# Kernel tuning notes

Hardware: AMD Instinct MI355X
Metric: run time of the kernel (lower is better)

## Reference

```python
import jax, jax.numpy as jnp
import numpy as np

SEQ = 4096
HIDDEN = 4096
HEAD_DIM = 1024
NUM_HEAD = HIDDEN // HEAD_DIM  # 4


def setup_inputs() -> dict:
    key = jax.random.key(0)
    ks = jax.random.split(key, 7)
    scale = 1.0 / np.sqrt(HIDDEN)  # torch Linear default-ish init scale
    h = jax.random.normal(ks[0], (SEQ, HIDDEN), dtype=jnp.float32)
    Wq = jax.random.normal(ks[1], (NUM_HEAD, HIDDEN, HEAD_DIM), dtype=jnp.float32) * scale
    bq = jax.random.normal(ks[2], (NUM_HEAD, HEAD_DIM), dtype=jnp.float32) * scale
    Wk = jax.random.normal(ks[3], (NUM_HEAD, HIDDEN, HEAD_DIM), dtype=jnp.float32) * scale
    bk = jax.random.normal(ks[4], (NUM_HEAD, HEAD_DIM), dtype=jnp.float32) * scale
    Wv = jax.random.normal(ks[5], (NUM_HEAD, HIDDEN, HEAD_DIM), dtype=jnp.float32) * scale
    bv = jax.random.normal(ks[6], (NUM_HEAD, HEAD_DIM), dtype=jnp.float32) * scale
    return {"h": h, "Wq": Wq, "bq": bq, "Wk": Wk, "bk": bk, "Wv": Wv, "bv": bv}


def reference(h, Wq, bq, Wk, bk, Wv, bv):
    # Batched per-head projections: q/k/v [H, S, E]
    q = jnp.einsum('sd,hde->hse', h, Wq) + bq[:, None, :]
    k = jnp.einsum('sd,hde->hse', h, Wk) + bk[:, None, :]
    v = jnp.einsum('sd,hde->hse', h, Wv) + bv[:, None, :]
    # Full (non-causal) attention scores [H, S, S], scaled by sqrt(head_dim)
    s = jnp.einsum('hse,hte->hst', q, k) / jnp.sqrt(jnp.asarray(HEAD_DIM, h.dtype))
    p = jax.nn.softmax(s, axis=-1)
    out = jnp.einsum('hst,hte->hse', p, v)  # [H, S, E]
    # Concatenate heads along feature dim -> [S, H*E]
    return jnp.transpose(out, (1, 0, 2)).reshape(h.shape[0], -1)
```

## Files before the change

kernel.cpp:

```cpp
#include <hip/hip_runtime.h>

#define SEQ   4096
#define HID   4096
#define EDIM  1024
#define NHEAD 4

typedef __attribute__((ext_vector_type(8))) short short8;
typedef __attribute__((ext_vector_type(4))) float f32x4;

typedef const __attribute__((address_space(1))) void* gas_ptr;
typedef __attribute__((address_space(3))) void* las_ptr;
#define GLD16(g, l) __builtin_amdgcn_global_load_lds((gas_ptr)(g), (las_ptr)(l), 16, 0, 0)

#define BARRIER() __builtin_amdgcn_s_barrier()
#define SCHED0()  __builtin_amdgcn_sched_barrier(0)

__device__ __forceinline__ unsigned short f2bf(float f) {
  union { float f; unsigned u; } v; v.f = f;
  unsigned r = v.u + 0x7fffu + ((v.u >> 16) & 1u);
  return (unsigned short)(r >> 16);
}
__device__ __forceinline__ float bf2f(unsigned short u) {
  union { unsigned u; float f; } v; v.u = ((unsigned)u) << 16;
  return v.f;
}

__global__ __launch_bounds__(256) void hconv_kernel(const float* __restrict__ in,
                                                    unsigned short* __restrict__ out) {
  size_t i = ((size_t)blockIdx.x * 256 + threadIdx.x) * 8;
  const float4 a = *(const float4*)(in + i);
  const float4 b = *(const float4*)(in + i + 4);
  short8 o;
  o[0] = (short)f2bf(a.x); o[1] = (short)f2bf(a.y);
  o[2] = (short)f2bf(a.z); o[3] = (short)f2bf(a.w);
  o[4] = (short)f2bf(b.x); o[5] = (short)f2bf(b.y);
  o[6] = (short)f2bf(b.z); o[7] = (short)f2bf(b.w);
  *(short8*)(out + i) = o;
}

__global__ __launch_bounds__(256) void wconv_kernel(const float* __restrict__ Wq,
                                                    const float* __restrict__ Wk,
                                                    const float* __restrict__ Wv,
                                                    unsigned short* __restrict__ wt) {
  const int mh = blockIdx.y;
  const int mat = mh >> 2, head = mh & 3;
  const float* W = (mat == 0 ? Wq : (mat == 1 ? Wk : Wv)) + (size_t)head * HID * EDIM;
  unsigned short* out = wt + (size_t)mh * EDIM * HID;
  const int tile = blockIdx.x;
  const int td = tile >> 4;
  const int te = tile & 15;
  __shared__ float lds[64][65];
  const int tid = threadIdx.x;
  const int r = tid >> 4, c4 = (tid & 15) * 4;
#pragma unroll
  for (int it = 0; it < 4; ++it) {
    int dr = r + 16 * it;
    const float4 v = *(const float4*)&W[(size_t)(td * 64 + dr) * EDIM + te * 64 + c4];
    lds[dr][c4 + 0] = v.x; lds[dr][c4 + 1] = v.y;
    lds[dr][c4 + 2] = v.z; lds[dr][c4 + 3] = v.w;
  }
  __syncthreads();
#pragma unroll
  for (int it = 0; it < 4; ++it) {
    int er = r + 16 * it;
    ushort4 o;
    o.x = f2bf(lds[c4 + 0][er]); o.y = f2bf(lds[c4 + 1][er]);
    o.z = f2bf(lds[c4 + 2][er]); o.w = f2bf(lds[c4 + 3][er]);
    *(ushort4*)&out[(size_t)(te * 64 + er) * HID + td * 64 + c4] = o;
  }
}

template <int MODE>
__global__ __launch_bounds__(512, 2) void gemm256_kernel(
    const unsigned short* __restrict__ Aall, const unsigned short* __restrict__ Ball,
    long long aBatch, long long bBatch, int K,
    const float* __restrict__ biasAll, long long biasBatch,
    void* __restrict__ outAll, long long outBatch, int ldOut, float scale,
    int gx, int gxy) {
  extern __shared__ char smem[];

  const int nwg = (int)gridDim.x;
  const int lin = (int)blockIdx.x;
  int wg = (lin & 7) * (nwg >> 3) + (lin >> 3);
  const int z = wg / gxy; wg -= z * gxy;
  const int by = wg / gx;
  const int bx = wg - by * gx;
  const int bm = by * 256, bn = bx * 256;

  const unsigned short* A = Aall + (size_t)z * aBatch;
  const unsigned short* B = Ball + (size_t)z * bBatch;

  const int tid = threadIdx.x;
  const int lane = tid & 63, wid = tid >> 6;
  const int wr = wid >> 2, wc = wid & 3;
  const int li = lane & 15, lg = lane >> 4;

  const int r0 = tid >> 2, s0 = tid & 3;
  const int kx = (s0 ^ ((r0 >> 1) & 3)) * 8;
  const unsigned short* aS0 = A + (size_t)(bm + r0) * K + kx;
  const unsigned short* aS1 = A + (size_t)(bm + r0 + 128) * K + kx;
  const unsigned short* bS0 = B + (size_t)(bn + r0) * K + kx;
  const unsigned short* bS1 = B + (size_t)(bn + r0 + 128) * K + kx;
  char* dA0 = smem + tid * 16;
  char* dA1 = smem + tid * 16 + 8192;
  char* dB0 = smem + 16384 + tid * 16;
  char* dB1 = smem + 16384 + tid * 16 + 8192;

  const int swz = (li >> 1) & 3;
  const int aOff = (wr * 128 + li) * 64 + ((lg ^ swz) * 16);
  const int bOff = 16384 + (wc * 64 + li) * 64 + ((lg ^ swz) * 16);

  f32x4 acc[8][4];
#pragma unroll
  for (int m = 0; m < 8; ++m)
#pragma unroll
    for (int n = 0; n < 4; ++n) acc[m][n] = (f32x4){0.f, 0.f, 0.f, 0.f};

  const int NT = K >> 5;

  for (int t = 0; t < 3; ++t) {
    const int rg = (t & 3) * 32768;
    GLD16(aS0 + (size_t)t * 32, dA0 + rg);
    GLD16(aS1 + (size_t)t * 32, dA1 + rg);
    GLD16(bS0 + (size_t)t * 32, dB0 + rg);
    GLD16(bS1 + (size_t)t * 32, dB1 + rg);
  }
  asm volatile("s_waitcnt vmcnt(8)" ::: "memory");
  BARRIER();
  SCHED0();

  for (int t = 0; t < NT; ++t) {
    const char* base = smem + (t & 3) * 32768;
    short8 av[8], bv[4];
#pragma unroll
    for (int m = 0; m < 4; ++m) av[m] = *(const short8*)(base + aOff + m * 1024);
#pragma unroll
    for (int n = 0; n < 4; ++n) bv[n] = *(const short8*)(base + bOff + n * 1024);
    if (t + 3 < NT) {
      const int rg = ((t + 3) & 3) * 32768;
      GLD16(aS0 + (size_t)(t + 3) * 32, dA0 + rg);
      GLD16(aS1 + (size_t)(t + 3) * 32, dA1 + rg);
    }
    SCHED0();
    BARRIER();
    asm volatile("s_waitcnt lgkmcnt(0)" ::: "memory");
    SCHED0();
    __builtin_amdgcn_s_setprio(1);
#pragma unroll
    for (int m = 0; m < 4; ++m)
#pragma unroll
      for (int n = 0; n < 4; ++n)
        acc[m][n] = __builtin_amdgcn_mfma_f32_16x16x32_bf16(av[m], bv[n], acc[m][n], 0, 0, 0);
    __builtin_amdgcn_s_setprio(0);
    SCHED0();
    BARRIER();
    SCHED0();
#pragma unroll
    for (int m = 4; m < 8; ++m) av[m] = *(const short8*)(base + aOff + m * 1024);
    if (t + 3 < NT) {
      const int rg = ((t + 3) & 3) * 32768;
      GLD16(bS0 + (size_t)(t + 3) * 32, dB0 + rg);
      GLD16(bS1 + (size_t)(t + 3) * 32, dB1 + rg);
    }
    if (t < NT - 3) {
      asm volatile("s_waitcnt vmcnt(8)" ::: "memory");
    } else if (t == NT - 3) {
      asm volatile("s_waitcnt vmcnt(4)" ::: "memory");
    } else if (t == NT - 2) {
      asm volatile("s_waitcnt vmcnt(0)" ::: "memory");
    }
    SCHED0();
    BARRIER();
    asm volatile("s_waitcnt lgkmcnt(0)" ::: "memory");
    SCHED0();
    __builtin_amdgcn_s_setprio(1);
#pragma unroll
    for (int m = 4; m < 8; ++m)
#pragma unroll
      for (int n = 0; n < 4; ++n)
        acc[m][n] = __builtin_amdgcn_mfma_f32_16x16x32_bf16(av[m], bv[n], acc[m][n], 0, 0, 0);
    __builtin_amdgcn_s_setprio(0);
    SCHED0();
    BARRIER();
    SCHED0();
  }

  float bvv[4];
  if (MODE == 0 || MODE == 1) {
    const float* bias = biasAll + (size_t)z * biasBatch;
#pragma unroll
    for (int n = 0; n < 4; ++n) bvv[n] = bias[bn + wc * 64 + n * 16 + li];
  }
#pragma unroll
  for (int m = 0; m < 8; ++m)
#pragma unroll
    for (int n = 0; n < 4; ++n)
#pragma unroll
      for (int r = 0; r < 4; ++r) {
        const int grow = bm + wr * 128 + m * 16 + lg * 4 + r;
        const int gcol = bn + wc * 64 + n * 16 + li;
        float val = acc[m][n][r];
        if (MODE == 0 || MODE == 1) val += bvv[n];
        if (MODE == 2) val *= scale;
        if (MODE == 0 || MODE == 2) {
          unsigned short* o = (unsigned short*)outAll + (size_t)z * outBatch;
          o[(size_t)grow * ldOut + gcol] = f2bf(val);
        } else if (MODE == 1) {
          unsigned short* o = (unsigned short*)outAll + (size_t)z * outBatch;
          o[(size_t)gcol * ldOut + grow] = f2bf(val);
        } else {
          float* o = (float*)outAll + (size_t)z * outBatch;
          o[(size_t)grow * ldOut + gcol] = val;
        }
      }
}

__global__ __launch_bounds__(256) void softmax_kernel(unsigned short* __restrict__ Sb) {
  const size_t row = blockIdx.x;
  unsigned short* p = Sb + row * (size_t)SEQ;
  const int tid = threadIdx.x;
  const int lane = tid & 63, wid = tid >> 6;
  float v[16];
  const short8 u0 = *(const short8*)&p[tid * 16];
  const short8 u1 = *(const short8*)&p[tid * 16 + 8];
#pragma unroll
  for (int j = 0; j < 8; ++j) v[j] = bf2f((unsigned short)u0[j]);
#pragma unroll
  for (int j = 0; j < 8; ++j) v[8 + j] = bf2f((unsigned short)u1[j]);
  float mx = v[0];
#pragma unroll
  for (int j = 1; j < 16; ++j) mx = fmaxf(mx, v[j]);
#pragma unroll
  for (int off = 32; off; off >>= 1) mx = fmaxf(mx, __shfl_xor(mx, off));
  __shared__ float red[8];
  if (lane == 0) red[wid] = mx;
  __syncthreads();
  mx = fmaxf(fmaxf(red[0], red[1]), fmaxf(red[2], red[3]));
  float s = 0.f;
#pragma unroll
  for (int j = 0; j < 16; ++j) { v[j] = __expf(v[j] - mx); s += v[j]; }
#pragma unroll
  for (int off = 32; off; off >>= 1) s += __shfl_xor(s, off);
  if (lane == 0) red[4 + wid] = s;
  __syncthreads();
  s = (red[4] + red[5]) + (red[6] + red[7]);
  const float inv = 1.0f / s;
  short8 o0, o1;
#pragma unroll
  for (int j = 0; j < 8; ++j) o0[j] = (short)f2bf(v[j] * inv);
#pragma unroll
  for (int j = 0; j < 8; ++j) o1[j] = (short)f2bf(v[8 + j] * inv);
  *(short8*)&p[tid * 16] = o0;
  *(short8*)&p[tid * 16 + 8] = o1;
}

extern "C" void kernel_launch(void* const* d_in, const int* in_sizes, int n_in,
                              void* d_out, int out_size, void* d_ws, size_t ws_size,
                              hipStream_t stream) {
  const float* h  = (const float*)d_in[0];
  const float* Wq = (const float*)d_in[1];
  const float* bq = (const float*)d_in[2];
  const float* Wk = (const float*)d_in[3];
  const float* bk = (const float*)d_in[4];
  const float* Wv = (const float*)d_in[5];
  const float* bv = (const float*)d_in[6];
  float* out = (float*)d_out;
  char* ws = (char*)d_ws;

  (void)hipFuncSetAttribute((const void*)&gemm256_kernel<0>,
                            hipFuncAttributeMaxDynamicSharedMemorySize, 131072);
  (void)hipFuncSetAttribute((const void*)&gemm256_kernel<1>,
                            hipFuncAttributeMaxDynamicSharedMemorySize, 131072);
  (void)hipFuncSetAttribute((const void*)&gemm256_kernel<2>,
                            hipFuncAttributeMaxDynamicSharedMemorySize, 131072);
  (void)hipFuncSetAttribute((const void*)&gemm256_kernel<3>,
                            hipFuncAttributeMaxDynamicSharedMemorySize, 131072);

  unsigned short* hB = (unsigned short*)ws;
  unsigned short* wt = (unsigned short*)(ws + (32ull << 20));
  unsigned short* Sb = (unsigned short*)ws;
  unsigned short* Qb = (unsigned short*)(ws + (128ull << 20));
  unsigned short* Kb = (unsigned short*)(ws + (160ull << 20));
  unsigned short* Vt = (unsigned short*)(ws + (192ull << 20));

  const long long WED = (long long)EDIM * HID;
  const long long QKB = (long long)SEQ * EDIM;
  const long long SSB = (long long)SEQ * SEQ;

  hconv_kernel<<<dim3((SEQ * (size_t)HID) / (256 * 8)), 256, 0, stream>>>(h, hB);
  wconv_kernel<<<dim3((HID / 64) * (EDIM / 64), 12), 256, 0, stream>>>(Wq, Wk, Wv, wt);

  gemm256_kernel<0><<<dim3(4 * 16 * 4), 512, 131072, stream>>>(
      hB, wt + 0 * WED, 0, WED, HID, bq, EDIM, Qb, QKB, EDIM, 1.f, 4, 64);
  gemm256_kernel<0><<<dim3(4 * 16 * 4), 512, 131072, stream>>>(
      hB, wt + 4 * WED, 0, WED, HID, bk, EDIM, Kb, QKB, EDIM, 1.f, 4, 64);
  gemm256_kernel<1><<<dim3(4 * 16 * 4), 512, 131072, stream>>>(
      hB, wt + 8 * WED, 0, WED, HID, bv, EDIM, Vt, QKB, SEQ, 1.f, 4, 64);

  gemm256_kernel<2><<<dim3(16 * 16 * 4), 512, 131072, stream>>>(
      Qb, Kb, QKB, QKB, EDIM, nullptr, 0, Sb, SSB, SEQ, 0.03125f, 16, 256);

  softmax_kernel<<<dim3(NHEAD * SEQ), 256, 0, stream>>>(Sb);

  gemm256_kernel<3><<<dim3(4 * 16 * 4), 512, 131072, stream>>>(
      Sb, Vt, SSB, QKB, SEQ, nullptr, 0, out, (long long)EDIM, NHEAD * EDIM, 1.f, 4, 64);
}
```

Before: 769.0 us.

## Restructure GEMM main loop to K=64 tiles with double-buffered quarter-tile pipeline

The bf16 MFMA GEMM main loop moves from 32-wide K tiles in a 4-stage LDS ring to 64-wide K tiles in two 64KB buffers. Each buffer is split into A/B halves that are refilled in quarters, interleaved with eight MFMA phases per iteration pair. The LDS swizzle changes to an 8-way XOR over 128-byte rows. The aim is fewer barriers per unit of K, more MFMAs per LDS read phase, and finer overlap of global-to-LDS loads with compute. In exchange it adds more complex waitcnt bookkeeping, higher register pressure from the 2x K fragments, and assumes NT is even.

```diff
diff --git a/kernel.cpp b/kernel.cpp
--- a/kernel.cpp
+++ b/kernel.cpp
@@ -95,20 +95,28 @@
   const int wr = wid >> 2, wc = wid & 3;
   const int li = lane & 15, lg = lane >> 4;
 
-  const int r0 = tid >> 2, s0 = tid & 3;
-  const int kx = (s0 ^ ((r0 >> 1) & 3)) * 8;
-  const unsigned short* aS0 = A + (size_t)(bm + r0) * K + kx;
-  const unsigned short* aS1 = A + (size_t)(bm + r0 + 128) * K + kx;
-  const unsigned short* bS0 = B + (size_t)(bn + r0) * K + kx;
-  const unsigned short* bS1 = B + (size_t)(bn + r0 + 128) * K + kx;
-  char* dA0 = smem + tid * 16;
-  char* dA1 = smem + tid * 16 + 8192;
-  char* dB0 = smem + 16384 + tid * 16;
-  char* dB1 = smem + 16384 + tid * 16 + 8192;
-
-  const int swz = (li >> 1) & 3;
-  const int aOff = (wr * 128 + li) * 64 + ((lg ^ swz) * 16);
-  const int bOff = 16384 + (wc * 64 + li) * 64 + ((lg ^ swz) * 16);
+  const int srow = tid >> 3;
+  const int sk = ((tid & 7) ^ (srow & 7)) * 8;
+  const unsigned short* aS00 = A + (size_t)(bm +   0 + srow) * K + sk;
+  const unsigned short* aS01 = A + (size_t)(bm +  64 + srow) * K + sk;
+  const unsigned short* aS10 = A + (size_t)(bm + 128 + srow) * K + sk;
+  const unsigned short* aS11 = A + (size_t)(bm + 192 + srow) * K + sk;
+  const unsigned short* bS00 = B + (size_t)(bn +   0 + srow) * K + sk;
+  const unsigned short* bS01 = B + (size_t)(bn +  64 + srow) * K + sk;
+  const unsigned short* bS10 = B + (size_t)(bn + 128 + srow) * K + sk;
+  const unsigned short* bS11 = B + (size_t)(bn + 192 + srow) * K + sk;
+
+#define STG(p0, p1, regionOff, tt)                                        \
+  do {                                                                    \
+    char* _d = smem + (((tt) & 1) << 16) + (regionOff) + tid * 16;        \
+    GLD16((p0) + (size_t)(tt) * 64, _d);                                  \
+    GLD16((p1) + (size_t)(tt) * 64, _d + 8192);                           \
+  } while (0)
+
+  const int aBase = (wr * 128 + li) * 128;
+  const int bBase = 32768 + (wc * 64 + li) * 128;
+  const int axk0 = ((0 + lg) ^ (li & 7)) * 16;
+  const int axk1 = ((4 + lg) ^ (li & 7)) * 16;
 
   f32x4 acc[8][4];
 #pragma unroll
@@ -116,74 +124,211 @@
 #pragma unroll
     for (int n = 0; n < 4; ++n) acc[m][n] = (f32x4){0.f, 0.f, 0.f, 0.f};
 
-  const int NT = K >> 5;
-
-  for (int t = 0; t < 3; ++t) {
-    const int rg = (t & 3) * 32768;
-    GLD16(aS0 + (size_t)t * 32, dA0 + rg);
-    GLD16(aS1 + (size_t)t * 32, dA1 + rg);
-    GLD16(bS0 + (size_t)t * 32, dB0 + rg);
-    GLD16(bS1 + (size_t)t * 32, dB1 + rg);
-  }
-  asm volatile("s_waitcnt vmcnt(8)" ::: "memory");
+  const int NT = K >> 6;
+  const int NI = NT >> 1;
+
+  STG(aS00, aS01, 0, 0);
+  STG(aS10, aS11, 16384, 0);
+  STG(bS00, bS01, 32768, 0);
+  STG(bS10, bS11, 49152, 0);
+  STG(bS00, bS01, 32768, 1);
+  STG(bS10, bS11, 49152, 1);
+  asm volatile("s_waitcnt vmcnt(4)" ::: "memory");
   BARRIER();
   SCHED0();
 
-  for (int t = 0; t < NT; ++t) {
-    const char* base = smem + (t & 3) * 32768;
-    short8 av[8], bv[4];
-#pragma unroll
-    for (int m = 0; m < 4; ++m) av[m] = *(const short8*)(base + aOff + m * 1024);
-#pragma unroll
-    for (int n = 0; n < 4; ++n) bv[n] = *(const short8*)(base + bOff + n * 1024);
+  short8 av[4][2], bv[4][2];
+
+  for (int i = 0; i < NI; ++i) {
+    const int t = 2 * i;
+    const char* s0 = smem;
+    const char* s1 = smem + 65536;
+
+#pragma unroll
+    for (int m = 0; m < 4; ++m) {
+      av[m][0] = *(const short8*)(s0 + aBase + m * 2048 + axk0);
+      av[m][1] = *(const short8*)(s0 + aBase + m * 2048 + axk1);
+    }
+#pragma unroll
+    for (int n = 0; n < 2; ++n) {
+      bv[n][0] = *(const short8*)(s0 + bBase + n * 2048 + axk0);
+      bv[n][1] = *(const short8*)(s0 + bBase + n * 2048 + axk1);
+    }
+    STG(aS00, aS01, 0, t + 1);
+    asm volatile("s_waitcnt lgkmcnt(8)" ::: "memory");
+    SCHED0();
+    BARRIER();
+    asm volatile("s_waitcnt lgkmcnt(0)" ::: "memory");
+    SCHED0();
+    __builtin_amdgcn_s_setprio(1);
+#pragma unroll
+    for (int m = 0; m < 4; ++m)
+#pragma unroll
+      for (int n = 0; n < 2; ++n) {
+        acc[m][n] = __builtin_amdgcn_mfma_f32_16x16x32_bf16(av[m][0], bv[n][0], acc[m][n], 0, 0, 0);
+        acc[m][n] = __builtin_amdgcn_mfma_f32_16x16x32_bf16(av[m][1], bv[n][1], acc[m][n], 0, 0, 0);
+      }
+    __builtin_amdgcn_s_setprio(0);
+    SCHED0();
+    BARRIER();
+
+#pragma unroll
+    for (int n = 2; n < 4; ++n) {
+      bv[n][0] = *(const short8*)(s0 + bBase + n * 2048 + axk0);
+      bv[n][1] = *(const short8*)(s0 + bBase + n * 2048 + axk1);
+    }
+    STG(aS10, aS11, 16384, t + 1);
+    SCHED0();
+    BARRIER();
+    asm volatile("s_waitcnt lgkmcnt(0)" ::: "memory");
+    SCHED0();
+    __builtin_amdgcn_s_setprio(1);
+#pragma unroll
+    for (int m = 0; m < 4; ++m)
+#pragma unroll
+      for (int n = 2; n < 4; ++n) {
+        acc[m][n] = __builtin_amdgcn_mfma_f32_16x16x32_bf16(av[m][0], bv[n][0], acc[m][n], 0, 0, 0);
+        acc[m][n] = __builtin_amdgcn_mfma_f32_16x16x32_bf16(av[m][1], bv[n][1], acc[m][n], 0, 0, 0);
+      }
+    __builtin_amdgcn_s_setprio(0);
+    SCHED0();
+    BARRIER();
+
+#pragma unroll
+    for (int m = 0; m < 4; ++m) {
+      av[m][0] = *(const short8*)(s0 + aBase + (m + 4) * 2048 + axk0);
+      av[m][1] = *(const short8*)(s0 + aBase + (m + 4) * 2048 + axk1);
+    }
+    if (t + 2 < NT) STG(bS00, bS01, 32768, t + 2);
+    SCHED0();
+    BARRIER();
+    asm volatile("s_waitcnt lgkmcnt(0)" ::: "memory");
+    SCHED0();
+    __builtin_amdgcn_s_setprio(1);
+#pragma unroll
+    for (int m = 0; m < 4; ++m)
+#pragma unroll
+      for (int n = 0; n < 2; ++n) {
+        acc[m + 4][n] = __builtin_amdgcn_mfma_f32_16x16x32_bf16(av[m][0], bv[n][0], acc[m + 4][n], 0, 0, 0);
+        acc[m + 4][n] = __builtin_amdgcn_mfma_f32_16x16x32_bf16(av[m][1], bv[n][1], acc[m + 4][n], 0, 0, 0);
+      }
+    __builtin_amdgcn_s_setprio(0);
+    SCHED0();
+    BARRIER();
+
+    if (t + 2 < NT) {
+      STG(bS10, bS11, 49152, t + 2);
+      asm volatile("s_waitcnt vmcnt(4)" ::: "memory");
+    } else {
+      asm volatile("s_waitcnt vmcnt(0)" ::: "memory");
+    }
+    SCHED0();
+    BARRIER();
+    __builtin_amdgcn_s_setprio(1);
+#pragma unroll
+    for (int m = 0; m < 4; ++m)
+#pragma unroll
+      for (int n = 2; n < 4; ++n) {
+        acc[m + 4][n] = __builtin_amdgcn_mfma_f32_16x16x32_bf16(av[m][0], bv[n][0], acc[m + 4][n], 0, 0, 0);
+        acc[m + 4][n] = __builtin_amdgcn_mfma_f32_16x16x32_bf16(av[m][1], bv[n][1], acc[m + 4][n], 0, 0, 0);
+      }
+    __builtin_amdgcn_s_setprio(0);
+    SCHED0();
+    BARRIER();
+
+#pragma unroll
+    for (int m = 0; m < 4; ++m) {
+      av[m][0] = *(const short8*)(s1 + aBase + m * 2048 + axk0);
+      av[m][1] = *(const short8*)(s1 + aBase + m * 2048 + axk1);
+    }
+#pragma unroll
+    for (int n = 0; n < 2; ++n) {
+      bv[n][0] = *(const short8*)(s1 + bBase + n * 2048 + axk0);
+      bv[n][1] = *(const short8*)(s1 + bBase + n * 2048 + axk1);
+    }
+    if (t + 2 < NT) STG(aS00, aS01, 0, t + 2);
+    asm volatile("s_waitcnt lgkmcnt(8)" ::: "memory");
+    SCHED0();
+    BARRIER();
+    asm volatile("s_waitcnt lgkmcnt(0)" ::: "memory");
+    SCHED0();
+    __builtin_amdgcn_s_setprio(1);
+#pragma unroll
+    for (int m = 0; m < 4; ++m)
+#pragma unroll
+      for (int n = 0; n < 2; ++n) {
+        acc[m][n] = __builtin_amdgcn_mfma_f32_16x16x32_bf16(av[m][0], bv[n][0], acc[m][n], 0, 0, 0);
+        acc[m][n] = __builtin_amdgcn_mfma_f32_16x16x32_bf16(av[m][1], bv[n][1], acc[m][n], 0, 0, 0);
+      }
+    __builtin_amdgcn_s_setprio(0);
+    SCHED0();
+    BARRIER();
+
+#pragma unroll
+    for (int n = 2; n < 4; ++n) {
+      bv[n][0] = *(const short8*)(s1 + bBase + n * 2048 + axk0);
+      bv[n][1] = *(const short8*)(s1 + bBase + n * 2048 + axk1);
+    }
+    if (t + 2 < NT) STG(aS10, aS11, 16384, t + 2);
+    SCHED0();
+    BARRIER();
+    asm volatile("s_waitcnt lgkmcnt(0)" ::: "memory");
+    SCHED0();
+    __builtin_amdgcn_s_setprio(1);
+#pragma unroll
+    for (int m = 0; m < 4; ++m)
+#pragma unroll
+      for (int n = 2; n < 4; ++n) {
+        acc[m][n] = __builtin_amdgcn_mfma_f32_16x16x32_bf16(av[m][0], bv[n][0], acc[m][n], 0, 0, 0);
+        acc[m][n] = __builtin_amdgcn_mfma_f32_16x16x32_bf16(av[m][1], bv[n][1], acc[m][n], 0, 0, 0);
+      }
+    __builtin_amdgcn_s_setprio(0);
+    SCHED0();
+    BARRIER();
+
+#pragma unroll
+    for (int m = 0; m < 4; ++m) {
+      av[m][0] = *(const short8*)(s1 + aBase + (m + 4) * 2048 + axk0);
+      av[m][1] = *(const short8*)(s1 + aBase + (m + 4) * 2048 + axk1);
+    }
+    if (t + 3 < NT) STG(bS00, bS01, 32768, t + 3);
+    SCHED0();
+    BARRIER();
+    asm volatile("s_waitcnt lgkmcnt(0)" ::: "memory");
+    SCHED0();
+    __builtin_amdgcn_s_setprio(1);
+#pragma unroll
+    for (int m = 0; m < 4; ++m)
+#pragma unroll
+      for (int n = 0; n < 2; ++n) {
+        acc[m + 4][n] = __builtin_amdgcn_mfma_f32_16x16x32_bf16(av[m][0], bv[n][0], acc[m + 4][n], 0, 0, 0);
+        acc[m + 4][n] = __builtin_amdgcn_mfma_f32_16x16x32_bf16(av[m][1], bv[n][1], acc[m + 4][n], 0, 0, 0);
+      }
+    __builtin_amdgcn_s_setprio(0);
+    SCHED0();
+    BARRIER();
+
     if (t + 3 < NT) {
-      const int rg = ((t + 3) & 3) * 32768;
-      GLD16(aS0 + (size_t)(t + 3) * 32, dA0 + rg);
-      GLD16(aS1 + (size_t)(t + 3) * 32, dA1 + rg);
-    }
-    SCHED0();
-    BARRIER();
-    asm volatile("s_waitcnt lgkmcnt(0)" ::: "memory");
-    SCHED0();
-    __builtin_amdgcn_s_setprio(1);
-#pragma unroll
-    for (int m = 0; m < 4; ++m)
-#pragma unroll
-      for (int n = 0; n < 4; ++n)
-        acc[m][n] = __builtin_amdgcn_mfma_f32_16x16x32_bf16(av[m], bv[n], acc[m][n], 0, 0, 0);
-    __builtin_amdgcn_s_setprio(0);
-    SCHED0();
-    BARRIER();
-    SCHED0();
-#pragma unroll
-    for (int m = 4; m < 8; ++m) av[m] = *(const short8*)(base + aOff + m * 1024);
-    if (t + 3 < NT) {
-      const int rg = ((t + 3) & 3) * 32768;
-      GLD16(bS0 + (size_t)(t + 3) * 32, dB0 + rg);
-      GLD16(bS1 + (size_t)(t + 3) * 32, dB1 + rg);
-    }
-    if (t < NT - 3) {
-      asm volatile("s_waitcnt vmcnt(8)" ::: "memory");
-    } else if (t == NT - 3) {
+      STG(bS10, bS11, 49152, t + 3);
       asm volatile("s_waitcnt vmcnt(4)" ::: "memory");
-    } else if (t == NT - 2) {
+    } else {
       asm volatile("s_waitcnt vmcnt(0)" ::: "memory");
     }
     SCHED0();
     BARRIER();
-    asm volatile("s_waitcnt lgkmcnt(0)" ::: "memory");
-    SCHED0();
-    __builtin_amdgcn_s_setprio(1);
-#pragma unroll
-    for (int m = 4; m < 8; ++m)
-#pragma unroll
-      for (int n = 0; n < 4; ++n)
-        acc[m][n] = __builtin_amdgcn_mfma_f32_16x16x32_bf16(av[m], bv[n], acc[m][n], 0, 0, 0);
-    __builtin_amdgcn_s_setprio(0);
-    SCHED0();
-    BARRIER();
-    SCHED0();
+    __builtin_amdgcn_s_setprio(1);
+#pragma unroll
+    for (int m = 0; m < 4; ++m)
+#pragma unroll
+      for (int n = 2; n < 4; ++n) {
+        acc[m + 4][n] = __builtin_amdgcn_mfma_f32_16x16x32_bf16(av[m][0], bv[n][0], acc[m + 4][n], 0, 0, 0);
+        acc[m + 4][n] = __builtin_amdgcn_mfma_f32_16x16x32_bf16(av[m][1], bv[n][1], acc[m + 4][n], 0, 0, 0);
+      }
+    __builtin_amdgcn_s_setprio(0);
+    SCHED0();
+    BARRIER();
   }
+#undef STG
 
   float bvv[4];
   if (MODE == 0 || MODE == 1) {
```

New measurement: 717.0 us. 1.07x faster.

## Switch GEMM to 32x32x16 MFMA with 64-wide K tiles and double buffering

Applied to the files above, without the earlier changes.

Replaces the 16x16x32 MFMA tiling with 32x32x16 bf16 MFMA instructions. Each K step now covers 64 elements, using a two-stage double-buffered LDS pipeline in place of the four-deep ring of 32-wide slices. The LDS layout uses a new XOR swizzle over 128-byte rows, and the epilogue is remapped to the 32x32 accumulator layout. The aim is fewer LDS reads and fewer MFMA issues per FLOP, at the cost of a shallower prefetch depth and a larger per-stage LDS footprint.

```diff
diff --git a/kernel.cpp b/kernel.cpp
--- a/kernel.cpp
+++ b/kernel.cpp
@@ -6,7 +6,7 @@
 #define NHEAD 4
 
 typedef __attribute__((ext_vector_type(8))) short short8;
-typedef __attribute__((ext_vector_type(4))) float f32x4;
+typedef __attribute__((ext_vector_type(16))) float f32x16;
 
 typedef const __attribute__((address_space(1))) void* gas_ptr;
 typedef __attribute__((address_space(3))) void* las_ptr;
@@ -14,6 +14,8 @@
 
 #define BARRIER() __builtin_amdgcn_s_barrier()
 #define SCHED0()  __builtin_amdgcn_sched_barrier(0)
+#define LGKM0()   asm volatile("s_waitcnt lgkmcnt(0)" ::: "memory")
+#define VMC(N)    asm volatile("s_waitcnt vmcnt(" #N ")" ::: "memory")
 
 __device__ __forceinline__ unsigned short f2bf(float f) {
   union { float f; unsigned u; } v; v.f = f;
@@ -93,112 +95,139 @@
   const int tid = threadIdx.x;
   const int lane = tid & 63, wid = tid >> 6;
   const int wr = wid >> 2, wc = wid & 3;
-  const int li = lane & 15, lg = lane >> 4;
-
-  const int r0 = tid >> 2, s0 = tid & 3;
-  const int kx = (s0 ^ ((r0 >> 1) & 3)) * 8;
-  const unsigned short* aS0 = A + (size_t)(bm + r0) * K + kx;
-  const unsigned short* aS1 = A + (size_t)(bm + r0 + 128) * K + kx;
-  const unsigned short* bS0 = B + (size_t)(bn + r0) * K + kx;
-  const unsigned short* bS1 = B + (size_t)(bn + r0 + 128) * K + kx;
-  char* dA0 = smem + tid * 16;
-  char* dA1 = smem + tid * 16 + 8192;
-  char* dB0 = smem + 16384 + tid * 16;
-  char* dB1 = smem + 16384 + tid * 16 + 8192;
-
-  const int swz = (li >> 1) & 3;
-  const int aOff = (wr * 128 + li) * 64 + ((lg ^ swz) * 16);
-  const int bOff = 16384 + (wc * 64 + li) * 64 + ((lg ^ swz) * 16);
-
-  f32x4 acc[8][4];
-#pragma unroll
-  for (int m = 0; m < 8; ++m)
-#pragma unroll
-    for (int n = 0; n < 4; ++n) acc[m][n] = (f32x4){0.f, 0.f, 0.f, 0.f};
-
-  const int NT = K >> 5;
-
-  for (int t = 0; t < 3; ++t) {
-    const int rg = (t & 3) * 32768;
-    GLD16(aS0 + (size_t)t * 32, dA0 + rg);
-    GLD16(aS1 + (size_t)t * 32, dA1 + rg);
-    GLD16(bS0 + (size_t)t * 32, dB0 + rg);
-    GLD16(bS1 + (size_t)t * 32, dB1 + rg);
-  }
-  asm volatile("s_waitcnt vmcnt(8)" ::: "memory");
+  const int la31 = lane & 31, lg2 = lane >> 5;
+
+  const int srow = tid >> 3;
+  const int sk = ((tid & 7) ^ ((srow ^ (srow >> 3)) & 7)) * 8;
+  const unsigned short* aS00 = A + (size_t)(bm +   0 + srow) * K + sk;
+  const unsigned short* aS01 = A + (size_t)(bm +  64 + srow) * K + sk;
+  const unsigned short* aS10 = A + (size_t)(bm + 128 + srow) * K + sk;
+  const unsigned short* aS11 = A + (size_t)(bm + 192 + srow) * K + sk;
+  const unsigned short* bS00 = B + (size_t)(bn +   0 + srow) * K + sk;
+  const unsigned short* bS01 = B + (size_t)(bn +  64 + srow) * K + sk;
+  const unsigned short* bS10 = B + (size_t)(bn + 128 + srow) * K + sk;
+  const unsigned short* bS11 = B + (size_t)(bn + 192 + srow) * K + sk;
+
+#define STG(p0, p1, regionOff, tt)                                        \
+  do {                                                                    \
+    char* _d = smem + (((tt) & 1) << 16) + (regionOff) + tid * 16;        \
+    GLD16((p0) + (size_t)(tt) * 64, _d);                                  \
+    GLD16((p1) + (size_t)(tt) * 64, _d + 8192);                           \
+  } while (0)
+
+  int aO[4], aX[4];
+#pragma unroll
+  for (int m = 0; m < 4; ++m) {
+    const int arow = wr * 128 + m * 32 + la31;
+    aO[m] = arow * 128;
+    aX[m] = (arow ^ (arow >> 3)) & 7;
+  }
+  int bO[2], bX[2];
+#pragma unroll
+  for (int n = 0; n < 2; ++n) {
+    const int brow = wc * 64 + n * 32 + la31;
+    bO[n] = 32768 + brow * 128;
+    bX[n] = (brow ^ (brow >> 3)) & 7;
+  }
+
+  f32x16 acc[4][2];
+#pragma unroll
+  for (int m = 0; m < 4; ++m)
+#pragma unroll
+    for (int n = 0; n < 2; ++n)
+#pragma unroll
+      for (int r = 0; r < 16; ++r) acc[m][n][r] = 0.f;
+
+  const int NT = K >> 6;
+
+  STG(aS00, aS01, 0, 0);
+  STG(aS10, aS11, 16384, 0);
+  STG(bS00, bS01, 32768, 0);
+  STG(bS10, bS11, 49152, 0);
+  STG(bS00, bS01, 32768, 1);
+  STG(bS10, bS11, 49152, 1);
+  VMC(4);
   BARRIER();
-  SCHED0();
+
+  short8 av[2][4], bv[2][4];
 
   for (int t = 0; t < NT; ++t) {
-    const char* base = smem + (t & 3) * 32768;
-    short8 av[8], bv[4];
-#pragma unroll
-    for (int m = 0; m < 4; ++m) av[m] = *(const short8*)(base + aOff + m * 1024);
-#pragma unroll
-    for (int n = 0; n < 4; ++n) bv[n] = *(const short8*)(base + bOff + n * 1024);
-    if (t + 3 < NT) {
-      const int rg = ((t + 3) & 3) * 32768;
-      GLD16(aS0 + (size_t)(t + 3) * 32, dA0 + rg);
-      GLD16(aS1 + (size_t)(t + 3) * 32, dA1 + rg);
+    const char* base = smem + ((t & 1) << 16);
+
+#pragma unroll
+    for (int m = 0; m < 2; ++m)
+#pragma unroll
+      for (int ks = 0; ks < 4; ++ks)
+        av[m][ks] = *(const short8*)(base + aO[m] + ((((ks << 1) + lg2) ^ aX[m]) << 4));
+#pragma unroll
+    for (int n = 0; n < 2; ++n)
+#pragma unroll
+      for (int ks = 0; ks < 4; ++ks)
+        bv[n][ks] = *(const short8*)(base + bO[n] + ((((ks << 1) + lg2) ^ bX[n]) << 4));
+    if (t + 1 < NT) {
+      STG(aS00, aS01, 0, t + 1);
+      STG(aS10, aS11, 16384, t + 1);
     }
-    SCHED0();
     BARRIER();
-    asm volatile("s_waitcnt lgkmcnt(0)" ::: "memory");
+    LGKM0();
     SCHED0();
     __builtin_amdgcn_s_setprio(1);
 #pragma unroll
-    for (int m = 0; m < 4; ++m)
-#pragma unroll
-      for (int n = 0; n < 4; ++n)
-        acc[m][n] = __builtin_amdgcn_mfma_f32_16x16x32_bf16(av[m], bv[n], acc[m][n], 0, 0, 0);
+    for (int ks = 0; ks < 4; ++ks)
+#pragma unroll
+      for (int m = 0; m < 2; ++m)
+#pragma unroll
+        for (int n = 0; n < 2; ++n)
+          acc[m][n] = __builtin_amdgcn_mfma_f32_32x32x16_bf16(av[m][ks], bv[n][ks], acc[m][n], 0, 0, 0);
     __builtin_amdgcn_s_setprio(0);
     SCHED0();
     BARRIER();
-    SCHED0();
-#pragma unroll
-    for (int m = 4; m < 8; ++m) av[m] = *(const short8*)(base + aOff + m * 1024);
-    if (t + 3 < NT) {
-      const int rg = ((t + 3) & 3) * 32768;
-      GLD16(bS0 + (size_t)(t + 3) * 32, dB0 + rg);
-      GLD16(bS1 + (size_t)(t + 3) * 32, dB1 + rg);
+
+#pragma unroll
+    for (int m = 0; m < 2; ++m)
+#pragma unroll
+      for (int ks = 0; ks < 4; ++ks)
+        av[m][ks] = *(const short8*)(base + aO[m + 2] + ((((ks << 1) + lg2) ^ aX[m + 2]) << 4));
+    if (t + 2 < NT) {
+      STG(bS00, bS01, 32768, t + 2);
+      STG(bS10, bS11, 49152, t + 2);
     }
-    if (t < NT - 3) {
-      asm volatile("s_waitcnt vmcnt(8)" ::: "memory");
-    } else if (t == NT - 3) {
-      asm volatile("s_waitcnt vmcnt(4)" ::: "memory");
-    } else if (t == NT - 2) {
-      asm volatile("s_waitcnt vmcnt(0)" ::: "memory");
-    }
-    SCHED0();
     BARRIER();
-    asm volatile("s_waitcnt lgkmcnt(0)" ::: "memory");
+    LGKM0();
     SCHED0();
     __builtin_amdgcn_s_setprio(1);
 #pragma unroll
-    for (int m = 4; m < 8; ++m)
-#pragma unroll
-      for (int n = 0; n < 4; ++n)
-        acc[m][n] = __builtin_amdgcn_mfma_f32_16x16x32_bf16(av[m], bv[n], acc[m][n], 0, 0, 0);
+    for (int ks = 0; ks < 4; ++ks)
+#pragma unroll
+      for (int m = 0; m < 2; ++m)
+#pragma unroll
+        for (int n = 0; n < 2; ++n)
+          acc[m + 2][n] = __builtin_amdgcn_mfma_f32_32x32x16_bf16(av[m][ks], bv[n][ks], acc[m + 2][n], 0, 0, 0);
     __builtin_amdgcn_s_setprio(0);
     SCHED0();
+    if (t + 2 < NT) {
+      VMC(4);
+    } else {
+      VMC(0);
+    }
     BARRIER();
-    SCHED0();
-  }
-
-  float bvv[4];
+  }
+#undef STG
+
+  float bvv[2];
   if (MODE == 0 || MODE == 1) {
     const float* bias = biasAll + (size_t)z * biasBatch;
 #pragma unroll
-    for (int n = 0; n < 4; ++n) bvv[n] = bias[bn + wc * 64 + n * 16 + li];
-  }
-#pragma unroll
-  for (int m = 0; m < 8; ++m)
-#pragma unroll
-    for (int n = 0; n < 4; ++n)
-#pragma unroll
-      for (int r = 0; r < 4; ++r) {
-        const int grow = bm + wr * 128 + m * 16 + lg * 4 + r;
-        const int gcol = bn + wc * 64 + n * 16 + li;
+    for (int n = 0; n < 2; ++n) bvv[n] = bias[bn + wc * 64 + n * 32 + la31];
+  }
+#pragma unroll
+  for (int m = 0; m < 4; ++m)
+#pragma unroll
+    for (int n = 0; n < 2; ++n)
+#pragma unroll
+      for (int r = 0; r < 16; ++r) {
+        const int grow = bm + wr * 128 + m * 32 + (r & 3) + 8 * (r >> 2) + 4 * lg2;
+        const int gcol = bn + wc * 64 + n * 32 + la31;
         float val = acc[m][n][r];
         if (MODE == 0 || MODE == 1) val += bvv[n];
         if (MODE == 2) val *= scale;
```

Measured after the change: 783.1 us. Within noise of the previous version (+1.8%).
